# Performance work log

Hardware: AMD Instinct MI355X
Metric: run time of the kernel (lower is better)

Reference implementation:

```python
import jax, jax.numpy as jnp
import numpy as np

B, T, D = 2, 2048, 2048
N_HEADS, N_KV = 16, 4
HD = D // N_HEADS  # 128
ROPE_BASE = 10000.0


def _rope_tables(t, dim, base=ROPE_BASE):
    inv_freq = 1.0 / (base ** (jnp.arange(0, dim, 2, dtype=jnp.float32) / dim))
    freqs = jnp.arange(t, dtype=jnp.float32)[:, None] * inv_freq[None, :]  # (T, dim/2)
    emb = jnp.concatenate([freqs, freqs], axis=-1)  # (T, dim)
    return jnp.cos(emb), jnp.sin(emb)


def _rotate_half(x):
    x1, x2 = jnp.split(x, 2, axis=-1)
    return jnp.concatenate([-x2, x1], axis=-1)


def _apply_rope(x, cos, sin):
    # x: (B, H, T, hd); cos/sin: (T, hd)
    return x * cos[None, None] + _rotate_half(x) * sin[None, None]


def setup_inputs() -> dict:
    key = jax.random.key(0)
    ks = jax.random.split(key, 5)
    s = 0.02
    return {
        "x": jax.random.normal(ks[0], (B, T, D), jnp.float32),
        "wq": jax.random.normal(ks[1], (D, N_HEADS * HD), jnp.float32) * s,
        "wk": jax.random.normal(ks[2], (D, N_KV * HD), jnp.float32) * s,
        "wv": jax.random.normal(ks[3], (D, N_KV * HD), jnp.float32) * s,
        "wo": jax.random.normal(ks[4], (D, D), jnp.float32) * s,
    }


def reference(x, wq, wk, wv, wo):
    b, t, c = x.shape
    n_rep = N_HEADS // N_KV
    scale = 1.0 / np.sqrt(HD)

    q = (x @ wq).reshape(b, t, N_HEADS, HD).transpose(0, 2, 1, 3)  # (B,H,T,hd)
    k = (x @ wk).reshape(b, t, N_KV, HD).transpose(0, 2, 1, 3)     # (B,Hkv,T,hd)
    v = (x @ wv).reshape(b, t, N_KV, HD).transpose(0, 2, 1, 3)

    cos, sin = _rope_tables(t, HD)
    q = _apply_rope(q, cos, sin)
    k = _apply_rope(k, cos, sin)

    # repeat_kv (GQA)
    k = jnp.repeat(k, n_rep, axis=1)  # (B,H,T,hd)
    v = jnp.repeat(v, n_rep, axis=1)

    scores = jnp.einsum("bhqd,bhkd->bhqk", q, k) * scale
    causal = jnp.tril(jnp.ones((t, t), dtype=bool))
    scores = jnp.where(causal[None, None], scores, -jnp.inf)
    attn = jax.nn.softmax(scores, axis=-1)
    out = jnp.einsum("bhqk,bhkd->bhqd", attn, v)
    out = out.transpose(0, 2, 1, 3).reshape(b, t, c)
    return out @ wo
```

## Files before the change

### kernel.cpp

```cpp
#include <hip/hip_runtime.h>
#include <hip/hip_bf16.h>
#include <math.h>

#define B_   2
#define T_   2048
#define D_   2048
#define NH_  16
#define NKV_ 4
#define HD_  128
#define MROWS (B_*T_)
#define NQKV  (NH_*HD_ + 2*NKV_*HD_)

typedef __bf16 bf16_t;
typedef __bf16 bf16x8 __attribute__((ext_vector_type(8)));
typedef __bf16 bf16x4 __attribute__((ext_vector_type(4)));
typedef float  floatx4 __attribute__((ext_vector_type(4)));

__device__ __forceinline__ void async_copy16(const bf16_t* gsrc, bf16_t* ldst) {
  __builtin_amdgcn_global_load_lds(
      (const __attribute__((address_space(1))) unsigned int*)gsrc,
      (__attribute__((address_space(3))) unsigned int*)ldst, 16, 0, 0);
}

__global__ void cast_f32_bf16(const float* __restrict__ src, bf16_t* __restrict__ dst, int n) {
  int i = (blockIdx.x * 256 + threadIdx.x) * 8;
  if (i >= n) return;
  float4 a = *(const float4*)(src + i);
  float4 b = *(const float4*)(src + i + 4);
  bf16x8 v;
  v[0]=(bf16_t)a.x; v[1]=(bf16_t)a.y; v[2]=(bf16_t)a.z; v[3]=(bf16_t)a.w;
  v[4]=(bf16_t)b.x; v[5]=(bf16_t)b.y; v[6]=(bf16_t)b.z; v[7]=(bf16_t)b.w;
  *(bf16x8*)(dst + i) = v;
}

__global__ void transpose_cast(const float* __restrict__ src, bf16_t* __restrict__ dst,
                               int K, int N) {
  __shared__ float tile[32][33];
  int n0 = blockIdx.x * 32, k0 = blockIdx.y * 32;
  int tx = threadIdx.x, ty = threadIdx.y;
#pragma unroll
  for (int r = 0; r < 4; r++)
    tile[ty + r*8][tx] = src[(size_t)(k0 + ty + r*8) * N + n0 + tx];
  __syncthreads();
#pragma unroll
  for (int r = 0; r < 4; r++)
    dst[(size_t)(n0 + ty + r*8) * K + k0 + tx] = (bf16_t)tile[tx][ty + r*8];
}

template <typename OUT_T>
__global__ __launch_bounds__(256, 2)
void gemm_bt(const bf16_t* __restrict__ A, const bf16_t* __restrict__ Bt,
             OUT_T* __restrict__ C, int M, int N, int K) {
  __shared__ __align__(16) bf16_t As[128 * 64];
  __shared__ __align__(16) bf16_t Bs[128 * 64];
  const int tid  = threadIdx.x;
  const int wave = tid >> 6, lane = tid & 63;
  const int quad = lane >> 4, l16 = lane & 15;
  const int nBlocksM = M >> 7;
  const int bm = blockIdx.x % nBlocksM, bn = blockIdx.x / nBlocksM;
  const int m0 = bm * 128, n0 = bn * 128;
  const int wm = (wave >> 1) * 64, wn = (wave & 1) * 64;

  floatx4 acc[4][4];
#pragma unroll
  for (int i = 0; i < 4; i++)
#pragma unroll
    for (int j = 0; j < 4; j++) acc[i][j] = floatx4{0.f, 0.f, 0.f, 0.f};

  for (int k0 = 0; k0 < K; k0 += 64) {
    __syncthreads();
#pragma unroll
    for (int i = 0; i < 4; i++) {
      int e = i * 256 + tid;
      int row = e >> 3, grp = e & 7;
      int gg = grp ^ (row & 7);
      async_copy16(A + (size_t)(m0 + row) * K + k0 + gg * 8, As + e * 8);
    }
#pragma unroll
    for (int i = 0; i < 4; i++) {
      int e = i * 256 + tid;
      int row = e >> 3, grp = e & 7;
      int gg = grp ^ (row & 7);
      async_copy16(Bt + (size_t)(n0 + row) * K + k0 + gg * 8, Bs + e * 8);
    }
    __syncthreads();
#pragma unroll
    for (int ks = 0; ks < 2; ks++) {
      bf16x8 af[4], bfr[4];
      int grp = ks * 4 + quad;
#pragma unroll
      for (int mi = 0; mi < 4; mi++) {
        int row = wm + mi * 16 + l16;
        af[mi] = *(const bf16x8*)(As + row * 64 + ((grp ^ (row & 7)) << 3));
      }
#pragma unroll
      for (int ni = 0; ni < 4; ni++) {
        int row = wn + ni * 16 + l16;
        bfr[ni] = *(const bf16x8*)(Bs + row * 64 + ((grp ^ (row & 7)) << 3));
      }
#pragma unroll
      for (int mi = 0; mi < 4; mi++)
#pragma unroll
        for (int ni = 0; ni < 4; ni++)
          acc[mi][ni] = __builtin_amdgcn_mfma_f32_16x16x32_bf16(af[mi], bfr[ni], acc[mi][ni], 0, 0, 0);
    }
  }
#pragma unroll
  for (int mi = 0; mi < 4; mi++) {
#pragma unroll
    for (int r = 0; r < 4; r++) {
      int row = m0 + wm + mi * 16 + quad * 4 + r;
      size_t base = (size_t)row * N + n0 + wn;
#pragma unroll
      for (int ni = 0; ni < 4; ni++)
        C[base + ni * 16 + l16] = (OUT_T)acc[mi][ni][r];
    }
  }
}

__global__ void rope_scatter(const bf16_t* __restrict__ qkv,
                             bf16_t* __restrict__ Qb, bf16_t* __restrict__ Kb) {
  int g = blockIdx.x * 256 + threadIdx.x;
  int j = g & 63;
  int rest = g >> 6;
  int head = rest % (NH_ + NKV_);
  int row  = rest / (NH_ + NKV_);
  int t = row & (T_ - 1);
  int b = row >> 11;
  const bf16_t* src = qkv + (size_t)row * NQKV;
  float ang = (float)t * expf(-0.14391156816f * (float)j);
  float sn, cs;
  sincosf(ang, &sn, &cs);
  if (head < NH_) {
    float x0 = (float)src[head * HD_ + j];
    float x1 = (float)src[head * HD_ + 64 + j];
    const float scale = 0.12751651541057752f;
    bf16_t* dst = Qb + ((size_t)(b * NH_ + head) * T_ + t) * HD_;
    dst[j]      = (bf16_t)((x0 * cs - x1 * sn) * scale);
    dst[j + 64] = (bf16_t)((x1 * cs + x0 * sn) * scale);
  } else {
    int kvh = head - NH_;
    float x0 = (float)src[NH_ * HD_ + kvh * HD_ + j];
    float x1 = (float)src[NH_ * HD_ + kvh * HD_ + 64 + j];
    bf16_t* dst = Kb + ((size_t)(b * NKV_ + kvh) * T_ + t) * HD_;
    dst[j]      = (bf16_t)(x0 * cs - x1 * sn);
    dst[j + 64] = (bf16_t)(x1 * cs + x0 * sn);
  }
}

__global__ void v_transpose(const bf16_t* __restrict__ qkv, bf16_t* __restrict__ Vt) {
  __shared__ float tile[32][33];
  int t0 = blockIdx.x * 32, d0 = blockIdx.y * 32;
  int bk = blockIdx.z;
  int b = bk / NKV_, kvh = bk % NKV_;
  int tx = threadIdx.x, ty = threadIdx.y;
#pragma unroll
  for (int r = 0; r < 4; r++) {
    int t = t0 + ty + r * 8;
    tile[ty + r*8][tx] =
        (float)qkv[(size_t)(b * T_ + t) * NQKV + (NH_ + NKV_) * HD_ + kvh * HD_ + d0 + tx];
  }
  __syncthreads();
#pragma unroll
  for (int r = 0; r < 4; r++) {
    int d = d0 + ty + r * 8;
    Vt[((size_t)(b * NKV_ + kvh) * HD_ + d) * T_ + t0 + tx] = (bf16_t)tile[tx][ty + r*8];
  }
}

__global__ __launch_bounds__(256, 2)
void flash_attn(const bf16_t* __restrict__ Qb, const bf16_t* __restrict__ Kb,
                const bf16_t* __restrict__ Vt, bf16_t* __restrict__ Ob) {
  __shared__ __align__(16) bf16_t Ks[2][64 * 128];
  __shared__ __align__(16) bf16_t Vs[2][128 * 64];
  __shared__ __align__(16) bf16_t Ps[4][16 * 72];

  const int tid = threadIdx.x;
  const int wave = tid >> 6, lane = tid & 63;
  const int quad = lane >> 4, l16 = lane & 15;
  const int nQT = T_ / 64;
  const int bid = blockIdx.x;
  const int bh = bid % (B_ * NH_);
  const int qt = (nQT - 1) - (bid / (B_ * NH_));
  const int h = bh % NH_;
  const int b = bh / NH_;
  const int kv = h >> 2;

  const bf16_t* qbase = Qb + ((size_t)(b * NH_ + h) * T_ + qt * 64) * HD_;
  const bf16_t* kbase = Kb + ((size_t)(b * NKV_ + kv) * T_) * HD_;
  const bf16_t* vbase = Vt + ((size_t)(b * NKV_ + kv) * HD_) * T_;

  auto stage = [&](int kt, int bufi) {
#pragma unroll
    for (int i = 0; i < 4; i++) {
      int e = i * 256 + tid;
      int row = e >> 4, grp = e & 15;
      int gg = grp ^ (row & 15);
      async_copy16(kbase + (size_t)(kt * 64 + row) * HD_ + gg * 8, &Ks[bufi][e * 8]);
    }
#pragma unroll
    for (int i = 0; i < 4; i++) {
      int e = i * 256 + tid;
      int row = e >> 3, grp = e & 7;
      int gg = grp ^ (row & 7);
      async_copy16(vbase + (size_t)row * T_ + kt * 64 + gg * 8, &Vs[bufi][e * 8]);
    }
  };

  stage(0, 0);

  bf16x8 qf[4];
  {
    const bf16_t* qptr = qbase + (wave * 16 + l16) * HD_;
#pragma unroll
    for (int ks = 0; ks < 4; ks++)
      qf[ks] = *(const bf16x8*)(qptr + ks * 32 + quad * 8);
  }

  floatx4 o[8];
#pragma unroll
  for (int i = 0; i < 8; i++) o[i] = floatx4{0.f, 0.f, 0.f, 0.f};
  float m_s = -1e30f, l_s = 0.f;

  for (int kt = 0; kt <= qt; kt++) {
    const int bufi = kt & 1;
    __syncthreads();
    if (kt < qt) stage(kt + 1, bufi ^ 1);

    floatx4 s[4];
#pragma unroll
    for (int nt = 0; nt < 4; nt++) s[nt] = floatx4{0.f, 0.f, 0.f, 0.f};
#pragma unroll
    for (int ks = 0; ks < 4; ks++) {
      int grp = ks * 4 + quad;
#pragma unroll
      for (int nt = 0; nt < 4; nt++) {
        int row = nt * 16 + l16;
        bf16x8 kf = *(const bf16x8*)(&Ks[bufi][row * 128 + ((grp ^ (row & 15)) << 3)]);
        s[nt] = __builtin_amdgcn_mfma_f32_16x16x32_bf16(kf, qf[ks], s[nt], 0, 0, 0);
      }
    }

    if (kt == qt) {
      int qlocal = wave * 16 + l16;
#pragma unroll
      for (int nt = 0; nt < 4; nt++)
#pragma unroll
        for (int r = 0; r < 4; r++) {
          int klocal = nt * 16 + quad * 4 + r;
          if (klocal > qlocal) s[nt][r] = -1e30f;
        }
    }

    float mx = fmaxf(fmaxf(s[0][0], s[0][1]), fmaxf(s[0][2], s[0][3]));
#pragma unroll
    for (int nt = 1; nt < 4; nt++)
      mx = fmaxf(mx, fmaxf(fmaxf(s[nt][0], s[nt][1]), fmaxf(s[nt][2], s[nt][3])));
    mx = fmaxf(mx, __shfl_xor(mx, 16, 64));
    mx = fmaxf(mx, __shfl_xor(mx, 32, 64));
    float mnew = fmaxf(m_s, mx);
    float alpha = __builtin_amdgcn_exp2f(m_s - mnew);
    m_s = mnew;
    float sum = 0.f;
#pragma unroll
    for (int nt = 0; nt < 4; nt++)
#pragma unroll
      for (int r = 0; r < 4; r++) {
        float p = __builtin_amdgcn_exp2f(s[nt][r] - mnew);
        s[nt][r] = p;
        sum += p;
      }
    sum += __shfl_xor(sum, 16, 64);
    sum += __shfl_xor(sum, 32, 64);
    l_s = l_s * alpha + sum;
#pragma unroll
    for (int dt = 0; dt < 8; dt++) o[dt] *= alpha;

#pragma unroll
    for (int nt = 0; nt < 4; nt++) {
      bf16x4 p4;
#pragma unroll
      for (int r = 0; r < 4; r++) p4[r] = (bf16_t)s[nt][r];
      *(bf16x4*)(&Ps[wave][l16 * 72 + nt * 16 + quad * 4]) = p4;
    }

#pragma unroll
    for (int ks = 0; ks < 2; ks++) {
      bf16x8 pf = *(const bf16x8*)(&Ps[wave][l16 * 72 + ks * 32 + quad * 8]);
      int grp = ks * 4 + quad;
#pragma unroll
      for (int dt = 0; dt < 8; dt++) {
        int row = dt * 16 + l16;
        bf16x8 vf = *(const bf16x8*)(&Vs[bufi][row * 64 + ((grp ^ (row & 7)) << 3)]);
        o[dt] = __builtin_amdgcn_mfma_f32_16x16x32_bf16(vf, pf, o[dt], 0, 0, 0);
      }
    }
  }

  {
    int qg = qt * 64 + wave * 16 + l16;
    float inv_l = 1.f / l_s;
    size_t base = ((size_t)(b * T_) + qg) * D_ + h * HD_;
#pragma unroll
    for (int dt = 0; dt < 8; dt++) {
      bf16x4 w;
#pragma unroll
      for (int r = 0; r < 4; r++) w[r] = (bf16_t)(o[dt][r] * inv_l);
      *(bf16x4*)(Ob + base + dt * 16 + quad * 4) = w;
    }
  }
}

extern "C" void kernel_launch(void* const* d_in, const int* in_sizes, int n_in,
                              void* d_out, int out_size, void* d_ws, size_t ws_size,
                              hipStream_t stream) {
  const float* x  = (const float*)d_in[0];
  const float* wq = (const float*)d_in[1];
  const float* wk = (const float*)d_in[2];
  const float* wv = (const float*)d_in[3];
  const float* wo = (const float*)d_in[4];
  float* out = (float*)d_out;

  bf16_t* x_bf   = (bf16_t*)d_ws;
  bf16_t* attn_o = x_bf;
  bf16_t* wqkv_t = x_bf + (size_t)MROWS * D_;
  bf16_t* wo_t   = wqkv_t + (size_t)NQKV * D_;
  bf16_t* qkv    = wo_t + (size_t)D_ * D_;
  bf16_t* Qb     = qkv + (size_t)MROWS * NQKV;
  bf16_t* Kb     = Qb + (size_t)B_ * NH_ * T_ * HD_;
  bf16_t* Vt     = Kb + (size_t)B_ * NKV_ * T_ * HD_;

  cast_f32_bf16<<<(MROWS * D_) / (256 * 8), 256, 0, stream>>>(x, x_bf, MROWS * D_);
  transpose_cast<<<dim3(64, 64), dim3(32, 8), 0, stream>>>(wq, wqkv_t, D_, 2048);
  transpose_cast<<<dim3(16, 64), dim3(32, 8), 0, stream>>>(wk, wqkv_t + (size_t)2048 * D_, D_, 512);
  transpose_cast<<<dim3(16, 64), dim3(32, 8), 0, stream>>>(wv, wqkv_t + (size_t)2560 * D_, D_, 512);
  transpose_cast<<<dim3(64, 64), dim3(32, 8), 0, stream>>>(wo, wo_t, D_, 2048);

  gemm_bt<bf16_t><<<(MROWS / 128) * (NQKV / 128), 256, 0, stream>>>(
      x_bf, wqkv_t, qkv, MROWS, NQKV, D_);

  rope_scatter<<<(MROWS * (NH_ + NKV_) * 64) / 256, 256, 0, stream>>>(qkv, Qb, Kb);
  v_transpose<<<dim3(T_ / 32, HD_ / 32, B_ * NKV_), dim3(32, 8), 0, stream>>>(qkv, Vt);

  flash_attn<<<B_ * NH_ * (T_ / 64), 256, 0, stream>>>(Qb, Kb, Vt, attn_o);

  gemm_bt<float><<<(MROWS / 128) * (D_ / 128), 256, 0, stream>>>(
      attn_o, wo_t, out, MROWS, D_, D_);
}
```

Measured before the change: 280.5 us.

## Process two GQA heads per flash-attention block to share K/V tiles

Each flash-attention block now handles two query heads that share one KV head, so each K/V tile staged into LDS feeds twice the MFMA work and the grid shrinks by half. K/V staging pointers are precomputed and advanced incrementally instead of recomputed per tile. The output rescale by alpha is skipped when no lane's running max changed. The trade-off is higher register pressure from doubled Q fragments, accumulators and scores, which may reduce occupancy under the 2-block launch bound, plus fewer blocks to fill the GPU.

```diff
diff --git a/kernel.cpp b/kernel.cpp
--- a/kernel.cpp
+++ b/kernel.cpp
@@ -179,57 +179,73 @@
   const int wave = tid >> 6, lane = tid & 63;
   const int quad = lane >> 4, l16 = lane & 15;
   const int nQT = T_ / 64;
+  const int NPAIR = B_ * NKV_ * 2;
   const int bid = blockIdx.x;
-  const int bh = bid % (B_ * NH_);
-  const int qt = (nQT - 1) - (bid / (B_ * NH_));
-  const int h = bh % NH_;
-  const int b = bh / NH_;
-  const int kv = h >> 2;
-
-  const bf16_t* qbase = Qb + ((size_t)(b * NH_ + h) * T_ + qt * 64) * HD_;
+  const int pair = bid % NPAIR;
+  const int qt = (nQT - 1) - (bid / NPAIR);
+  const int hp = pair & 1;
+  const int bkv = pair >> 1;
+  const int kv = bkv % NKV_;
+  const int b = bkv / NKV_;
+  const int h0 = kv * 4 + hp * 2;
+
   const bf16_t* kbase = Kb + ((size_t)(b * NKV_ + kv) * T_) * HD_;
   const bf16_t* vbase = Vt + ((size_t)(b * NKV_ + kv) * HD_) * T_;
 
-  auto stage = [&](int kt, int bufi) {
+  const bf16_t* kptr[4];
+  const bf16_t* vptr[4];
+#pragma unroll
+  for (int i = 0; i < 4; i++) {
+    int e = i * 256 + tid;
+    { int row = e >> 4, grp = e & 15; int gg = grp ^ (row & 15);
+      kptr[i] = kbase + (size_t)row * HD_ + gg * 8; }
+    { int row = e >> 3, grp = e & 7;  int gg = grp ^ (row & 7);
+      vptr[i] = vbase + (size_t)row * T_ + gg * 8; }
+  }
+
+  auto stage = [&](int bufi) {
 #pragma unroll
     for (int i = 0; i < 4; i++) {
-      int e = i * 256 + tid;
-      int row = e >> 4, grp = e & 15;
-      int gg = grp ^ (row & 15);
-      async_copy16(kbase + (size_t)(kt * 64 + row) * HD_ + gg * 8, &Ks[bufi][e * 8]);
+      async_copy16(kptr[i], &Ks[bufi][(i * 256 + tid) * 8]);
+      kptr[i] += 64 * HD_;
     }
 #pragma unroll
     for (int i = 0; i < 4; i++) {
-      int e = i * 256 + tid;
-      int row = e >> 3, grp = e & 7;
-      int gg = grp ^ (row & 7);
-      async_copy16(vbase + (size_t)row * T_ + kt * 64 + gg * 8, &Vs[bufi][e * 8]);
+      async_copy16(vptr[i], &Vs[bufi][(i * 256 + tid) * 8]);
+      vptr[i] += 64;
     }
   };
 
-  stage(0, 0);
-
-  bf16x8 qf[4];
-  {
-    const bf16_t* qptr = qbase + (wave * 16 + l16) * HD_;
+  stage(0);
+
+  bf16x8 qf[2][4];
+#pragma unroll
+  for (int hd = 0; hd < 2; hd++) {
+    const bf16_t* qptr =
+        Qb + ((size_t)(b * NH_ + h0 + hd) * T_ + qt * 64 + wave * 16 + l16) * HD_;
 #pragma unroll
     for (int ks = 0; ks < 4; ks++)
-      qf[ks] = *(const bf16x8*)(qptr + ks * 32 + quad * 8);
-  }
-
-  floatx4 o[8];
-#pragma unroll
-  for (int i = 0; i < 8; i++) o[i] = floatx4{0.f, 0.f, 0.f, 0.f};
-  float m_s = -1e30f, l_s = 0.f;
+      qf[hd][ks] = *(const bf16x8*)(qptr + ks * 32 + quad * 8);
+  }
+
+  floatx4 o[2][8];
+#pragma unroll
+  for (int hd = 0; hd < 2; hd++)
+#pragma unroll
+    for (int i = 0; i < 8; i++) o[hd][i] = floatx4{0.f, 0.f, 0.f, 0.f};
+  float m_s[2] = {-1e30f, -1e30f};
+  float l_s[2] = {0.f, 0.f};
 
   for (int kt = 0; kt <= qt; kt++) {
     const int bufi = kt & 1;
     __syncthreads();
-    if (kt < qt) stage(kt + 1, bufi ^ 1);
-
-    floatx4 s[4];
-#pragma unroll
-    for (int nt = 0; nt < 4; nt++) s[nt] = floatx4{0.f, 0.f, 0.f, 0.f};
+    if (kt < qt) stage(bufi ^ 1);
+
+    floatx4 s[2][4];
+#pragma unroll
+    for (int hd = 0; hd < 2; hd++)
+#pragma unroll
+      for (int nt = 0; nt < 4; nt++) s[hd][nt] = floatx4{0.f, 0.f, 0.f, 0.f};
 #pragma unroll
     for (int ks = 0; ks < 4; ks++) {
       int grp = ks * 4 + quad;
@@ -237,7 +253,8 @@
       for (int nt = 0; nt < 4; nt++) {
         int row = nt * 16 + l16;
         bf16x8 kf = *(const bf16x8*)(&Ks[bufi][row * 128 + ((grp ^ (row & 15)) << 3)]);
-        s[nt] = __builtin_amdgcn_mfma_f32_16x16x32_bf16(kf, qf[ks], s[nt], 0, 0, 0);
+        s[0][nt] = __builtin_amdgcn_mfma_f32_16x16x32_bf16(kf, qf[0][ks], s[0][nt], 0, 0, 0);
+        s[1][nt] = __builtin_amdgcn_mfma_f32_16x16x32_bf16(kf, qf[1][ks], s[1][nt], 0, 0, 0);
       }
     }
 
@@ -248,64 +265,74 @@
 #pragma unroll
         for (int r = 0; r < 4; r++) {
           int klocal = nt * 16 + quad * 4 + r;
-          if (klocal > qlocal) s[nt][r] = -1e30f;
+          if (klocal > qlocal) { s[0][nt][r] = -1e30f; s[1][nt][r] = -1e30f; }
         }
     }
 
-    float mx = fmaxf(fmaxf(s[0][0], s[0][1]), fmaxf(s[0][2], s[0][3]));
-#pragma unroll
-    for (int nt = 1; nt < 4; nt++)
-      mx = fmaxf(mx, fmaxf(fmaxf(s[nt][0], s[nt][1]), fmaxf(s[nt][2], s[nt][3])));
-    mx = fmaxf(mx, __shfl_xor(mx, 16, 64));
-    mx = fmaxf(mx, __shfl_xor(mx, 32, 64));
-    float mnew = fmaxf(m_s, mx);
-    float alpha = __builtin_amdgcn_exp2f(m_s - mnew);
-    m_s = mnew;
-    float sum = 0.f;
-#pragma unroll
-    for (int nt = 0; nt < 4; nt++)
-#pragma unroll
-      for (int r = 0; r < 4; r++) {
-        float p = __builtin_amdgcn_exp2f(s[nt][r] - mnew);
-        s[nt][r] = p;
-        sum += p;
-      }
-    sum += __shfl_xor(sum, 16, 64);
-    sum += __shfl_xor(sum, 32, 64);
-    l_s = l_s * alpha + sum;
-#pragma unroll
-    for (int dt = 0; dt < 8; dt++) o[dt] *= alpha;
-
-#pragma unroll
-    for (int nt = 0; nt < 4; nt++) {
-      bf16x4 p4;
-#pragma unroll
-      for (int r = 0; r < 4; r++) p4[r] = (bf16_t)s[nt][r];
-      *(bf16x4*)(&Ps[wave][l16 * 72 + nt * 16 + quad * 4]) = p4;
-    }
-
-#pragma unroll
-    for (int ks = 0; ks < 2; ks++) {
-      bf16x8 pf = *(const bf16x8*)(&Ps[wave][l16 * 72 + ks * 32 + quad * 8]);
-      int grp = ks * 4 + quad;
-#pragma unroll
-      for (int dt = 0; dt < 8; dt++) {
-        int row = dt * 16 + l16;
-        bf16x8 vf = *(const bf16x8*)(&Vs[bufi][row * 64 + ((grp ^ (row & 7)) << 3)]);
-        o[dt] = __builtin_amdgcn_mfma_f32_16x16x32_bf16(vf, pf, o[dt], 0, 0, 0);
-      }
-    }
-  }
-
-  {
+#pragma unroll
+    for (int hd = 0; hd < 2; hd++) {
+      float mx = fmaxf(fmaxf(s[hd][0][0], s[hd][0][1]), fmaxf(s[hd][0][2], s[hd][0][3]));
+#pragma unroll
+      for (int nt = 1; nt < 4; nt++)
+        mx = fmaxf(mx, fmaxf(fmaxf(s[hd][nt][0], s[hd][nt][1]),
+                             fmaxf(s[hd][nt][2], s[hd][nt][3])));
+      mx = fmaxf(mx, __shfl_xor(mx, 16, 64));
+      mx = fmaxf(mx, __shfl_xor(mx, 32, 64));
+      float mold = m_s[hd];
+      float mnew = fmaxf(mold, mx);
+      m_s[hd] = mnew;
+      float sum = 0.f;
+#pragma unroll
+      for (int nt = 0; nt < 4; nt++)
+#pragma unroll
+        for (int r = 0; r < 4; r++) {
+          float p = __builtin_amdgcn_exp2f(s[hd][nt][r] - mnew);
+          s[hd][nt][r] = p;
+          sum += p;
+        }
+      sum += __shfl_xor(sum, 16, 64);
+      sum += __shfl_xor(sum, 32, 64);
+      if (__any(mnew > mold)) {
+        float alpha = __builtin_amdgcn_exp2f(mold - mnew);
+        l_s[hd] = l_s[hd] * alpha + sum;
+#pragma unroll
+        for (int dt = 0; dt < 8; dt++) o[hd][dt] *= alpha;
+      } else {
+        l_s[hd] += sum;
+      }
+
+#pragma unroll
+      for (int nt = 0; nt < 4; nt++) {
+        bf16x4 p4;
+#pragma unroll
+        for (int r = 0; r < 4; r++) p4[r] = (bf16_t)s[hd][nt][r];
+        *(bf16x4*)(&Ps[wave][l16 * 72 + nt * 16 + quad * 4]) = p4;
+      }
+
+#pragma unroll
+      for (int ks = 0; ks < 2; ks++) {
+        bf16x8 pf = *(const bf16x8*)(&Ps[wave][l16 * 72 + ks * 32 + quad * 8]);
+        int grp = ks * 4 + quad;
+#pragma unroll
+        for (int dt = 0; dt < 8; dt++) {
+          int row = dt * 16 + l16;
+          bf16x8 vf = *(const bf16x8*)(&Vs[bufi][row * 64 + ((grp ^ (row & 7)) << 3)]);
+          o[hd][dt] = __builtin_amdgcn_mfma_f32_16x16x32_bf16(vf, pf, o[hd][dt], 0, 0, 0);
+        }
+      }
+    }
+  }
+
+#pragma unroll
+  for (int hd = 0; hd < 2; hd++) {
     int qg = qt * 64 + wave * 16 + l16;
-    float inv_l = 1.f / l_s;
-    size_t base = ((size_t)(b * T_) + qg) * D_ + h * HD_;
+    float inv_l = 1.f / l_s[hd];
+    size_t base = ((size_t)(b * T_) + qg) * D_ + (h0 + hd) * HD_;
 #pragma unroll
     for (int dt = 0; dt < 8; dt++) {
       bf16x4 w;
 #pragma unroll
-      for (int r = 0; r < 4; r++) w[r] = (bf16_t)(o[dt][r] * inv_l);
+      for (int r = 0; r < 4; r++) w[r] = (bf16_t)(o[hd][dt][r] * inv_l);
       *(bf16x4*)(Ob + base + dt * 16 + quad * 4) = w;
     }
   }
@@ -342,7 +369,7 @@
   rope_scatter<<<(MROWS * (NH_ + NKV_) * 64) / 256, 256, 0, stream>>>(qkv, Qb, Kb);
   v_transpose<<<dim3(T_ / 32, HD_ / 32, B_ * NKV_), dim3(32, 8), 0, stream>>>(qkv, Vt);
 
-  flash_attn<<<B_ * NH_ * (T_ / 64), 256, 0, stream>>>(Qb, Kb, Vt, attn_o);
+  flash_attn<<<B_ * NKV_ * 2 * (T_ / 64), 256, 0, stream>>>(Qb, Kb, Vt, attn_o);
 
   gemm_bt<float><<<(MROWS / 128) * (D_ / 128), 256, 0, stream>>>(
       attn_o, wo_t, out, MROWS, D_, D_);
```

Result: slower. 294.6 us (+5.0%).
